# Kernel optimization log

Measured on AMD Instinct MI355X. Metric: run time of the kernel, lower is better.

## Reference

```python
import jax, jax.numpy as jnp
import numpy as np

B, N, E, H = 2048, 256, 32, 64
DIN = N + 2 * E  # masked_x + self_emb + parent_emb


def _lin_init(k, fan_in, fan_out):
    return jax.random.normal(k, (fan_in, fan_out), jnp.float32) / np.sqrt(fan_in).astype(np.float32)


def setup_inputs() -> dict:
    key = jax.random.key(0)
    ks = jax.random.split(key, 8)
    return {
        "x": jax.random.normal(ks[0], (B, N), jnp.float32),
        "adjacency": jax.random.uniform(ks[1], (N, N), jnp.float32),
        "embeddings": 0.01 * jax.random.normal(ks[2], (N, E), jnp.float32),
        "W1": _lin_init(ks[3], DIN, H), "b1": jnp.zeros((H,), jnp.float32),
        "g1": jnp.ones((H,), jnp.float32), "bt1": jnp.zeros((H,), jnp.float32),
        "W2": _lin_init(ks[4], H, H), "b2": jnp.zeros((H,), jnp.float32),
        "g2": jnp.ones((H,), jnp.float32), "bt2": jnp.zeros((H,), jnp.float32),
        "W3": _lin_init(ks[5], H, 2), "b3": jnp.zeros((2,), jnp.float32),
    }


def _layernorm(h, g, b, eps=1e-5):
    m = h.mean(-1, keepdims=True)
    v = h.var(-1, keepdims=True)
    return (h - m) / jnp.sqrt(v + eps) * g + b


def _leaky_relu(h):
    return jnp.where(h >= 0, h, 0.2 * h)


def reference(x, adjacency, embeddings, W1, b1, g1, bt1, W2, b2, g2, bt2, W3, b3):
    b, n = x.shape
    e = embeddings.shape[1]
    # masked_x[b,i,j] = adjacency[j,i] * x[b,j]  (per-node parent masking, vectorized over i)
    masked = x[:, None, :] * adjacency.T[None, :, :]            # (B, N, N)
    self_emb = jnp.broadcast_to(embeddings[None], (b, n, e))    # (B, N, E)
    # parent_weights[:, i] = adjacency[:, i] / (sum + 1e-8); parent_emb_i = pw_i @ embeddings
    pw = adjacency / (adjacency.sum(axis=0, keepdims=True) + 1e-8)
    parent_emb = jnp.broadcast_to((pw.T @ embeddings)[None], (b, n, e))  # (B, N, E)
    inp = jnp.concatenate([masked, self_emb, parent_emb], axis=-1)       # (B, N, N+2E)
    h = _leaky_relu(_layernorm(inp @ W1 + b1, g1, bt1))
    h = _leaky_relu(_layernorm(h @ W2 + b2, g2, bt2))
    out = h @ W3 + b3                                            # (B, N, 2)
    return out[..., 0], out[..., 1]  # (means, log_stds), each (B, N)
```

## Files before the change

### kernel.cpp

```cpp
#include <hip/hip_runtime.h>
#include <hip/hip_bf16.h>

#define BB 2048
#define NN 256
#define EE 32
#define HH 64

typedef __attribute__((ext_vector_type(8))) short s16x8;
typedef __attribute__((ext_vector_type(4))) short s16x4;
typedef __attribute__((ext_vector_type(4))) float f32x4;

__device__ __forceinline__ unsigned short f32_to_bf16_rne(float f) {
    unsigned int u = __float_as_uint(f);
    unsigned int r = u + 0x7FFFu + ((u >> 16) & 1u);
    return (unsigned short)(r >> 16);
}
__device__ __forceinline__ float bf16_to_f32(unsigned short h) {
    return __uint_as_float(((unsigned int)h) << 16);
}

__global__ void prep_x(const float* __restrict__ x,
                       unsigned short* __restrict__ xh,
                       unsigned short* __restrict__ xl) {
    const int i4 = (blockIdx.x * 256 + threadIdx.x) * 4;
    const f32x4 v = *(const f32x4*)(x + i4);
    s16x4 hv, lv;
    #pragma unroll
    for (int q = 0; q < 4; ++q) {
        const unsigned short hb = f32_to_bf16_rne(v[q]);
        hv[q] = (short)hb;
        lv[q] = (short)f32_to_bf16_rne(v[q] - bf16_to_f32(hb));
    }
    *(s16x4*)(xh + i4) = hv;
    *(s16x4*)(xl + i4) = lv;
}

__global__ __launch_bounds__(256) void precompute_c(
    const float* __restrict__ A, const float* __restrict__ emb,
    const float* __restrict__ W1, const float* __restrict__ b1,
    float* __restrict__ c) {
    const int i = blockIdx.x;
    const int t = threadIdx.x;
    __shared__ float aS[NN];
    __shared__ float red[256];
    __shared__ float peS[EE];

    const float a_t = A[t * NN + i];
    aS[t] = a_t;
    red[t] = a_t;
    __syncthreads();
    #pragma unroll
    for (int s = 128; s > 0; s >>= 1) {
        if (t < s) red[t] += red[t + s];
        __syncthreads();
    }
    const float inv = 1.f / (red[0] + 1e-8f);

    const int e = t & 31, jg = t >> 5;
    float part = 0.f;
    #pragma unroll 8
    for (int r = 0; r < 32; ++r) {
        const int j = jg * 32 + r;
        part = fmaf(aS[j], emb[j * EE + e], part);
    }
    __syncthreads();
    red[t] = part;
    __syncthreads();
    if (t < 32) {
        float pe = 0.f;
        #pragma unroll
        for (int g = 0; g < 8; ++g) pe += red[g * 32 + t];
        peS[t] = pe * inv;
    }
    __syncthreads();

    if (t < HH) {
        float ch = b1[t];
        const float* embi = emb + i * EE;
        #pragma unroll 8
        for (int e2 = 0; e2 < EE; ++e2) {
            ch = fmaf(embi[e2], W1[(NN      + e2) * HH + t], ch);
            ch = fmaf(peS[e2],  W1[(NN + EE + e2) * HH + t], ch);
        }
        c[i * HH + t] = ch;
    }
}

__global__ __launch_bounds__(256, 2) void fused_main(
    const unsigned short* __restrict__ xh, const unsigned short* __restrict__ xl,
    const float* __restrict__ A, const float* __restrict__ W1,
    const float* __restrict__ c,
    const float* __restrict__ g1, const float* __restrict__ bt1,
    const float* __restrict__ W2, const float* __restrict__ b2,
    const float* __restrict__ g2, const float* __restrict__ bt2,
    const float* __restrict__ W3, const float* __restrict__ b3,
    float* __restrict__ out) {

    __shared__ float smem[16384];
    __shared__ float aS[NN];
    unsigned short* Bh = (unsigned short*)smem;
    unsigned short* Bl = Bh + 32 * 512;
    float* h1 = smem;

    const int t  = threadIdx.x;
    const int i  = blockIdx.x & 255;
    const int b0 = (blockIdx.x >> 8) * 256;

    const int l  = t & 63;
    const int wv = t >> 6;
    const int lg = l >> 4;
    const int lm = l & 15;

    aS[t] = A[t * NN + i];
    __syncthreads();

    #pragma unroll
    for (int fr = 0; fr < 8; ++fr) {
        const int frag = wv * 8 + fr;
        const int kb = frag >> 2, nt = frag & 3;
        const int h  = nt * 16 + lm;
        const int jb = kb * 32 + lg * 8;
        s16x8 hv, lv;
        #pragma unroll
        for (int w = 0; w < 8; ++w) {
            const int j = jb + w;
            const float p = aS[j] * W1[j * HH + h];
            const unsigned short hb = f32_to_bf16_rne(p);
            hv[w] = (short)hb;
            lv[w] = (short)f32_to_bf16_rne(p - bf16_to_f32(hb));
        }
        *(s16x8*)(Bh + frag * 512 + l * 8) = hv;
        *(s16x8*)(Bl + frag * 512 + l * 8) = lv;
    }
    __syncthreads();

    f32x4 acc[4][4];
    #pragma unroll
    for (int rt = 0; rt < 4; ++rt)
        #pragma unroll
        for (int nt = 0; nt < 4; ++nt) {
            acc[rt][nt][0] = 0.f; acc[rt][nt][1] = 0.f;
            acc[rt][nt][2] = 0.f; acc[rt][nt][3] = 0.f;
        }

    const int rowbase = b0 + wv * 64;
    for (int kb = 0; kb < 8; ++kb) {
        s16x8 bh[4], bl[4];
        #pragma unroll
        for (int nt = 0; nt < 4; ++nt) {
            const int sbase = ((kb * 4 + nt) * 64 + l) * 8;
            bh[nt] = *(const s16x8*)(Bh + sbase);
            bl[nt] = *(const s16x8*)(Bl + sbase);
        }
        const int koff = kb * 32 + lg * 8;
        #pragma unroll
        for (int rt = 0; rt < 4; ++rt) {
            const int row = rowbase + rt * 16 + lm;
            const s16x8 ah = *(const s16x8*)(xh + row * NN + koff);
            const s16x8 al = *(const s16x8*)(xl + row * NN + koff);
            #pragma unroll
            for (int nt = 0; nt < 4; ++nt) {
                acc[rt][nt] = __builtin_amdgcn_mfma_f32_16x16x32_bf16(ah, bh[nt], acc[rt][nt], 0, 0, 0);
                acc[rt][nt] = __builtin_amdgcn_mfma_f32_16x16x32_bf16(ah, bl[nt], acc[rt][nt], 0, 0, 0);
                acc[rt][nt] = __builtin_amdgcn_mfma_f32_16x16x32_bf16(al, bh[nt], acc[rt][nt], 0, 0, 0);
            }
        }
    }
    __syncthreads();

    #pragma unroll
    for (int rt = 0; rt < 4; ++rt) {
        #pragma unroll
        for (int nt = 0; nt < 4; ++nt) {
            #pragma unroll
            for (int rr = 0; rr < 4; ++rr) {
                const int wr  = wv * 64 + rt * 16 + lg * 4 + rr;
                const int col = nt * 16 + lm;
                const int q   = col >> 2;
                h1[wr * 64 + (((q ^ (wr & 15)) << 2) | (col & 3))] = acc[rt][nt][rr];
            }
        }
    }
    __syncthreads();

    float acc1[HH];
    #pragma unroll
    for (int q = 0; q < 16; ++q) {
        const f32x4 v = *(const f32x4*)&h1[t * 64 + ((q ^ (t & 15)) << 2)];
        acc1[4*q+0] = v[0]; acc1[4*q+1] = v[1]; acc1[4*q+2] = v[2]; acc1[4*q+3] = v[3];
    }

    {
        const float* crow = c + i * HH;
        #pragma unroll
        for (int h = 0; h < HH; ++h) acc1[h] += crow[h];
    }

    {
        float m0 = 0.f, m1 = 0.f, m2 = 0.f, m3 = 0.f;
        #pragma unroll
        for (int h = 0; h < HH; h += 4) { m0 += acc1[h]; m1 += acc1[h+1]; m2 += acc1[h+2]; m3 += acc1[h+3]; }
        const float m = (m0 + m1 + m2 + m3) * (1.f / HH);
        float v0 = 0.f, v1 = 0.f, v2 = 0.f, v3 = 0.f;
        #pragma unroll
        for (int h = 0; h < HH; h += 4) {
            float d0 = acc1[h] - m, d1 = acc1[h+1] - m, d2 = acc1[h+2] - m, d3 = acc1[h+3] - m;
            v0 = fmaf(d0, d0, v0); v1 = fmaf(d1, d1, v1); v2 = fmaf(d2, d2, v2); v3 = fmaf(d3, d3, v3);
        }
        const float var = (v0 + v1 + v2 + v3) * (1.f / HH);
        const float inv = rsqrtf(var + 1e-5f);
        #pragma unroll
        for (int h = 0; h < HH; ++h) {
            float u = (acc1[h] - m) * inv * g1[h] + bt1[h];
            acc1[h] = (u >= 0.f) ? u : 0.2f * u;
        }
    }

    float acc2[HH];
    #pragma unroll
    for (int ho = 0; ho < HH; ++ho) acc2[ho] = b2[ho];
    #pragma unroll
    for (int h = 0; h < HH; ++h) {
        const float v = acc1[h];
        const float* w = W2 + h * HH;
        #pragma unroll
        for (int ho = 0; ho < HH; ++ho) acc2[ho] = fmaf(v, w[ho], acc2[ho]);
    }

    {
        float m0 = 0.f, m1 = 0.f, m2 = 0.f, m3 = 0.f;
        #pragma unroll
        for (int h = 0; h < HH; h += 4) { m0 += acc2[h]; m1 += acc2[h+1]; m2 += acc2[h+2]; m3 += acc2[h+3]; }
        const float m = (m0 + m1 + m2 + m3) * (1.f / HH);
        float v0 = 0.f, v1 = 0.f, v2 = 0.f, v3 = 0.f;
        #pragma unroll
        for (int h = 0; h < HH; h += 4) {
            float d0 = acc2[h] - m, d1 = acc2[h+1] - m, d2 = acc2[h+2] - m, d3 = acc2[h+3] - m;
            v0 = fmaf(d0, d0, v0); v1 = fmaf(d1, d1, v1); v2 = fmaf(d2, d2, v2); v3 = fmaf(d3, d3, v3);
        }
        const float var = (v0 + v1 + v2 + v3) * (1.f / HH);
        const float inv = rsqrtf(var + 1e-5f);
        #pragma unroll
        for (int h = 0; h < HH; ++h) {
            float u = (acc2[h] - m) * inv * g2[h] + bt2[h];
            acc2[h] = (u >= 0.f) ? u : 0.2f * u;
        }
    }

    float o0 = b3[0], o1 = b3[1];
    #pragma unroll
    for (int h = 0; h < HH; ++h) {
        o0 = fmaf(acc2[h], W3[h * 2 + 0], o0);
        o1 = fmaf(acc2[h], W3[h * 2 + 1], o1);
    }

    const int row = (b0 + t) * NN + i;
    out[row] = o0;
    out[BB * NN + row] = o1;
}

extern "C" void kernel_launch(void* const* d_in, const int* in_sizes, int n_in,
                              void* d_out, int out_size, void* d_ws, size_t ws_size,
                              hipStream_t stream) {
    const float* x   = (const float*)d_in[0];
    const float* A   = (const float*)d_in[1];
    const float* emb = (const float*)d_in[2];
    const float* W1  = (const float*)d_in[3];
    const float* b1  = (const float*)d_in[4];
    const float* g1  = (const float*)d_in[5];
    const float* bt1 = (const float*)d_in[6];
    const float* W2  = (const float*)d_in[7];
    const float* b2  = (const float*)d_in[8];
    const float* g2  = (const float*)d_in[9];
    const float* bt2 = (const float*)d_in[10];
    const float* W3  = (const float*)d_in[11];
    const float* b3  = (const float*)d_in[12];
    float* out = (float*)d_out;

    float* c = (float*)d_ws;
    unsigned short* xhp = (unsigned short*)(c + NN * HH);
    unsigned short* xlp = xhp + BB * NN;

    prep_x<<<(BB * NN) / 1024, 256, 0, stream>>>(x, xhp, xlp);
    precompute_c<<<NN, 256, 0, stream>>>(A, emb, W1, b1, c);
    fused_main<<<NN * (BB / 256), 256, 0, stream>>>(
        xhp, xlp, A, W1, c, g1, bt1, W2, b2, g2, bt2, W3, b3, out);
}
```

Measured before the change: 236.1 us.

## Split first GEMM into two 32-column halves to halve LDS and raise occupancy

The first-layer MFMA GEMM now runs in two passes over 32-column halves of the hidden dimension instead of one pass over all 64. This halves the shared-memory buffer and the per-thread accumulator tile, and the launch bounds go from 2 to 4 blocks per CU. The aim is more resident waves to hide the global loads of x. In exchange the xh/xl row tiles are loaded twice and there are extra barriers per block, and acc1[64] still adds register pressure that may cause spills under the tighter bound.

Result: slower. 379.1 us (+60.6%).

```diff
diff --git a/kernel.cpp b/kernel.cpp
--- a/kernel.cpp
+++ b/kernel.cpp
@@ -86,7 +86,7 @@
     }
 }
 
-__global__ __launch_bounds__(256, 2) void fused_main(
+__global__ __launch_bounds__(256, 4) void fused_main(
     const unsigned short* __restrict__ xh, const unsigned short* __restrict__ xl,
     const float* __restrict__ A, const float* __restrict__ W1,
     const float* __restrict__ c,
@@ -96,11 +96,11 @@
     const float* __restrict__ W3, const float* __restrict__ b3,
     float* __restrict__ out) {
 
-    __shared__ float smem[16384];
+    __shared__ float smem[8192];
     __shared__ float aS[NN];
     unsigned short* Bh = (unsigned short*)smem;
-    unsigned short* Bl = Bh + 32 * 512;
-    float* h1 = smem;
+    unsigned short* Bl = Bh + 16 * 512;
+    float* tr = smem;
 
     const int t  = threadIdx.x;
     const int i  = blockIdx.x & 255;
@@ -114,80 +114,86 @@
     aS[t] = A[t * NN + i];
     __syncthreads();
 
-    #pragma unroll
-    for (int fr = 0; fr < 8; ++fr) {
-        const int frag = wv * 8 + fr;
-        const int kb = frag >> 2, nt = frag & 3;
-        const int h  = nt * 16 + lm;
-        const int jb = kb * 32 + lg * 8;
-        s16x8 hv, lv;
-        #pragma unroll
-        for (int w = 0; w < 8; ++w) {
-            const int j = jb + w;
-            const float p = aS[j] * W1[j * HH + h];
-            const unsigned short hb = f32_to_bf16_rne(p);
-            hv[w] = (short)hb;
-            lv[w] = (short)f32_to_bf16_rne(p - bf16_to_f32(hb));
-        }
-        *(s16x8*)(Bh + frag * 512 + l * 8) = hv;
-        *(s16x8*)(Bl + frag * 512 + l * 8) = lv;
-    }
-    __syncthreads();
-
-    f32x4 acc[4][4];
-    #pragma unroll
-    for (int rt = 0; rt < 4; ++rt)
-        #pragma unroll
-        for (int nt = 0; nt < 4; ++nt) {
-            acc[rt][nt][0] = 0.f; acc[rt][nt][1] = 0.f;
-            acc[rt][nt][2] = 0.f; acc[rt][nt][3] = 0.f;
-        }
-
-    const int rowbase = b0 + wv * 64;
-    for (int kb = 0; kb < 8; ++kb) {
-        s16x8 bh[4], bl[4];
-        #pragma unroll
-        for (int nt = 0; nt < 4; ++nt) {
-            const int sbase = ((kb * 4 + nt) * 64 + l) * 8;
-            bh[nt] = *(const s16x8*)(Bh + sbase);
-            bl[nt] = *(const s16x8*)(Bl + sbase);
-        }
-        const int koff = kb * 32 + lg * 8;
+    float acc1[HH];
+
+    #pragma unroll
+    for (int p = 0; p < 2; ++p) {
+        #pragma unroll
+        for (int fr = 0; fr < 4; ++fr) {
+            const int f   = wv * 4 + fr;
+            const int kb  = f >> 1, ntl = f & 1;
+            const int h   = p * 32 + ntl * 16 + lm;
+            const int jb  = kb * 32 + lg * 8;
+            s16x8 hv, lv;
+            #pragma unroll
+            for (int w = 0; w < 8; ++w) {
+                const int j = jb + w;
+                const float pw = aS[j] * W1[j * HH + h];
+                const unsigned short hb = f32_to_bf16_rne(pw);
+                hv[w] = (short)hb;
+                lv[w] = (short)f32_to_bf16_rne(pw - bf16_to_f32(hb));
+            }
+            *(s16x8*)(Bh + f * 512 + l * 8) = hv;
+            *(s16x8*)(Bl + f * 512 + l * 8) = lv;
+        }
+        __syncthreads();
+
+        f32x4 acc[4][2];
+        #pragma unroll
+        for (int rt = 0; rt < 4; ++rt)
+            #pragma unroll
+            for (int n = 0; n < 2; ++n) {
+                acc[rt][n][0] = 0.f; acc[rt][n][1] = 0.f;
+                acc[rt][n][2] = 0.f; acc[rt][n][3] = 0.f;
+            }
+
+        const int rowbase = b0 + wv * 64;
+        for (int kb = 0; kb < 8; ++kb) {
+            s16x8 bh[2], bl[2];
+            #pragma unroll
+            for (int n = 0; n < 2; ++n) {
+                const int sbase = ((kb * 2 + n) * 64 + l) * 8;
+                bh[n] = *(const s16x8*)(Bh + sbase);
+                bl[n] = *(const s16x8*)(Bl + sbase);
+            }
+            const int koff = kb * 32 + lg * 8;
+            #pragma unroll
+            for (int rt = 0; rt < 4; ++rt) {
+                const int row = rowbase + rt * 16 + lm;
+                const s16x8 ah = *(const s16x8*)(xh + row * NN + koff);
+                const s16x8 al = *(const s16x8*)(xl + row * NN + koff);
+                #pragma unroll
+                for (int n = 0; n < 2; ++n) {
+                    acc[rt][n] = __builtin_amdgcn_mfma_f32_16x16x32_bf16(ah, bh[n], acc[rt][n], 0, 0, 0);
+                    acc[rt][n] = __builtin_amdgcn_mfma_f32_16x16x32_bf16(ah, bl[n], acc[rt][n], 0, 0, 0);
+                    acc[rt][n] = __builtin_amdgcn_mfma_f32_16x16x32_bf16(al, bh[n], acc[rt][n], 0, 0, 0);
+                }
+            }
+        }
+        __syncthreads();
+
         #pragma unroll
         for (int rt = 0; rt < 4; ++rt) {
-            const int row = rowbase + rt * 16 + lm;
-            const s16x8 ah = *(const s16x8*)(xh + row * NN + koff);
-            const s16x8 al = *(const s16x8*)(xl + row * NN + koff);
-            #pragma unroll
-            for (int nt = 0; nt < 4; ++nt) {
-                acc[rt][nt] = __builtin_amdgcn_mfma_f32_16x16x32_bf16(ah, bh[nt], acc[rt][nt], 0, 0, 0);
-                acc[rt][nt] = __builtin_amdgcn_mfma_f32_16x16x32_bf16(ah, bl[nt], acc[rt][nt], 0, 0, 0);
-                acc[rt][nt] = __builtin_amdgcn_mfma_f32_16x16x32_bf16(al, bh[nt], acc[rt][nt], 0, 0, 0);
-            }
-        }
-    }
-    __syncthreads();
-
-    #pragma unroll
-    for (int rt = 0; rt < 4; ++rt) {
-        #pragma unroll
-        for (int nt = 0; nt < 4; ++nt) {
-            #pragma unroll
-            for (int rr = 0; rr < 4; ++rr) {
-                const int wr  = wv * 64 + rt * 16 + lg * 4 + rr;
-                const int col = nt * 16 + lm;
-                const int q   = col >> 2;
-                h1[wr * 64 + (((q ^ (wr & 15)) << 2) | (col & 3))] = acc[rt][nt][rr];
-            }
-        }
-    }
-    __syncthreads();
-
-    float acc1[HH];
-    #pragma unroll
-    for (int q = 0; q < 16; ++q) {
-        const f32x4 v = *(const f32x4*)&h1[t * 64 + ((q ^ (t & 15)) << 2)];
-        acc1[4*q+0] = v[0]; acc1[4*q+1] = v[1]; acc1[4*q+2] = v[2]; acc1[4*q+3] = v[3];
+            #pragma unroll
+            for (int n = 0; n < 2; ++n) {
+                #pragma unroll
+                for (int rr = 0; rr < 4; ++rr) {
+                    const int wr  = wv * 64 + rt * 16 + lg * 4 + rr;
+                    const int col = n * 16 + lm;
+                    const int q   = col >> 2;
+                    tr[wr * 32 + (((q ^ (wr & 7)) << 2) | (col & 3))] = acc[rt][n][rr];
+                }
+            }
+        }
+        __syncthreads();
+
+        #pragma unroll
+        for (int g = 0; g < 8; ++g) {
+            const f32x4 v = *(const f32x4*)&tr[t * 32 + ((g ^ (t & 7)) << 2)];
+            acc1[p*32 + 4*g + 0] = v[0]; acc1[p*32 + 4*g + 1] = v[1];
+            acc1[p*32 + 4*g + 2] = v[2]; acc1[p*32 + 4*g + 3] = v[3];
+        }
+        __syncthreads();
     }
 
     {
```

## Move second-layer GEMM onto bf16 split-precision MFMA via shared-memory staging

Applied to the files above, without the earlier changes.

The per-thread scalar FP32 64x64 W2 matmul is replaced with MFMA bf16 hi/lo split (three products) computation. Layer-1 activations are split into bf16 hi/lo and written to LDS in MFMA fragment layout. A new prep kernel transposes and splits W2 once per call. The per-row LayerNorm epilogue is kept by transposing the accumulators back through LDS, which adds extra syncs and LDS traffic and slightly changes rounding.

Result: faster. 196.8 us (-16.6%).

```diff
diff --git a/kernel.cpp b/kernel.cpp
--- a/kernel.cpp
+++ b/kernel.cpp
@@ -33,6 +33,17 @@
     }
     *(s16x4*)(xh + i4) = hv;
     *(s16x4*)(xl + i4) = lv;
+}
+
+__global__ void prep_w2t(const float* __restrict__ W2,
+                         unsigned short* __restrict__ w2h,
+                         unsigned short* __restrict__ w2l) {
+    const int idx = blockIdx.x * 256 + threadIdx.x;
+    const int n = idx >> 6, k = idx & 63;
+    const float w = W2[k * HH + n];
+    const unsigned short hb = f32_to_bf16_rne(w);
+    w2h[n * HH + k] = hb;
+    w2l[n * HH + k] = f32_to_bf16_rne(w - bf16_to_f32(hb));
 }
 
 __global__ __launch_bounds__(256) void precompute_c(
@@ -90,8 +101,9 @@
     const unsigned short* __restrict__ xh, const unsigned short* __restrict__ xl,
     const float* __restrict__ A, const float* __restrict__ W1,
     const float* __restrict__ c,
+    const unsigned short* __restrict__ w2h, const unsigned short* __restrict__ w2l,
     const float* __restrict__ g1, const float* __restrict__ bt1,
-    const float* __restrict__ W2, const float* __restrict__ b2,
+    const float* __restrict__ b2,
     const float* __restrict__ g2, const float* __restrict__ bt2,
     const float* __restrict__ W3, const float* __restrict__ b3,
     float* __restrict__ out) {
@@ -100,7 +112,9 @@
     __shared__ float aS[NN];
     unsigned short* Bh = (unsigned short*)smem;
     unsigned short* Bl = Bh + 32 * 512;
-    float* h1 = smem;
+    float* tr = smem;
+    unsigned short* Ah = (unsigned short*)smem;
+    unsigned short* Al = Ah + 32 * 512;
 
     const int t  = threadIdx.x;
     const int i  = blockIdx.x & 255;
@@ -116,21 +130,21 @@
 
     #pragma unroll
     for (int fr = 0; fr < 8; ++fr) {
-        const int frag = wv * 8 + fr;
-        const int kb = frag >> 2, nt = frag & 3;
+        const int f  = wv * 8 + fr;
+        const int kb = f >> 2, nt = f & 3;
         const int h  = nt * 16 + lm;
         const int jb = kb * 32 + lg * 8;
         s16x8 hv, lv;
         #pragma unroll
         for (int w = 0; w < 8; ++w) {
             const int j = jb + w;
-            const float p = aS[j] * W1[j * HH + h];
-            const unsigned short hb = f32_to_bf16_rne(p);
+            const float pw = aS[j] * W1[j * HH + h];
+            const unsigned short hb = f32_to_bf16_rne(pw);
             hv[w] = (short)hb;
-            lv[w] = (short)f32_to_bf16_rne(p - bf16_to_f32(hb));
-        }
-        *(s16x8*)(Bh + frag * 512 + l * 8) = hv;
-        *(s16x8*)(Bl + frag * 512 + l * 8) = lv;
+            lv[w] = (short)f32_to_bf16_rne(pw - bf16_to_f32(hb));
+        }
+        *(s16x8*)(Bh + f * 512 + l * 8) = hv;
+        *(s16x8*)(Bl + f * 512 + l * 8) = lv;
     }
     __syncthreads();
 
@@ -169,33 +183,31 @@
     __syncthreads();
 
     #pragma unroll
-    for (int rt = 0; rt < 4; ++rt) {
-        #pragma unroll
-        for (int nt = 0; nt < 4; ++nt) {
+    for (int rt = 0; rt < 4; ++rt)
+        #pragma unroll
+        for (int nt = 0; nt < 4; ++nt)
             #pragma unroll
             for (int rr = 0; rr < 4; ++rr) {
                 const int wr  = wv * 64 + rt * 16 + lg * 4 + rr;
                 const int col = nt * 16 + lm;
                 const int q   = col >> 2;
-                h1[wr * 64 + (((q ^ (wr & 15)) << 2) | (col & 3))] = acc[rt][nt][rr];
-            }
-        }
-    }
+                tr[wr * 64 + (((q ^ (wr & 15)) << 2) | (col & 3))] = acc[rt][nt][rr];
+            }
     __syncthreads();
 
     float acc1[HH];
     #pragma unroll
     for (int q = 0; q < 16; ++q) {
-        const f32x4 v = *(const f32x4*)&h1[t * 64 + ((q ^ (t & 15)) << 2)];
+        const f32x4 v = *(const f32x4*)&tr[t * 64 + ((q ^ (t & 15)) << 2)];
         acc1[4*q+0] = v[0]; acc1[4*q+1] = v[1]; acc1[4*q+2] = v[2]; acc1[4*q+3] = v[3];
     }
+    __syncthreads();
 
     {
         const float* crow = c + i * HH;
         #pragma unroll
         for (int h = 0; h < HH; ++h) acc1[h] += crow[h];
     }
-
     {
         float m0 = 0.f, m1 = 0.f, m2 = 0.f, m3 = 0.f;
         #pragma unroll
@@ -216,42 +228,106 @@
         }
     }
 
-    float acc2[HH];
-    #pragma unroll
-    for (int ho = 0; ho < HH; ++ho) acc2[ho] = b2[ho];
-    #pragma unroll
-    for (int h = 0; h < HH; ++h) {
-        const float v = acc1[h];
-        const float* w = W2 + h * HH;
-        #pragma unroll
-        for (int ho = 0; ho < HH; ++ho) acc2[ho] = fmaf(v, w[ho], acc2[ho]);
-    }
+    {
+        const int f2base = (t >> 4) * 2;
+        const int lm2    = t & 15;
+        #pragma unroll
+        for (int w = 0; w < 8; ++w) {
+            const int kk = w >> 2, lg2 = w & 3;
+            s16x8 hv, lv;
+            #pragma unroll
+            for (int e = 0; e < 8; ++e) {
+                const float v = acc1[w * 8 + e];
+                const unsigned short hb = f32_to_bf16_rne(v);
+                hv[e] = (short)hb;
+                lv[e] = (short)f32_to_bf16_rne(v - bf16_to_f32(hb));
+            }
+            const int base = (f2base + kk) * 512 + (lg2 * 16 + lm2) * 8;
+            *(s16x8*)(Ah + base) = hv;
+            *(s16x8*)(Al + base) = lv;
+        }
+    }
+    __syncthreads();
+
+    f32x4 acc2[4][4];
+    #pragma unroll
+    for (int rt = 0; rt < 4; ++rt)
+        #pragma unroll
+        for (int nt = 0; nt < 4; ++nt) {
+            acc2[rt][nt][0] = 0.f; acc2[rt][nt][1] = 0.f;
+            acc2[rt][nt][2] = 0.f; acc2[rt][nt][3] = 0.f;
+        }
+    #pragma unroll
+    for (int kk = 0; kk < 2; ++kk) {
+        s16x8 b2h[4], b2l[4];
+        #pragma unroll
+        for (int nt = 0; nt < 4; ++nt) {
+            const int off = (nt * 16 + lm) * HH + kk * 32 + lg * 8;
+            b2h[nt] = *(const s16x8*)(w2h + off);
+            b2l[nt] = *(const s16x8*)(w2l + off);
+        }
+        #pragma unroll
+        for (int rt = 0; rt < 4; ++rt) {
+            const int base = ((wv * 4 + rt) * 2 + kk) * 512 + l * 8;
+            const s16x8 a2h = *(const s16x8*)(Ah + base);
+            const s16x8 a2l = *(const s16x8*)(Al + base);
+            #pragma unroll
+            for (int nt = 0; nt < 4; ++nt) {
+                acc2[rt][nt] = __builtin_amdgcn_mfma_f32_16x16x32_bf16(a2h, b2h[nt], acc2[rt][nt], 0, 0, 0);
+                acc2[rt][nt] = __builtin_amdgcn_mfma_f32_16x16x32_bf16(a2h, b2l[nt], acc2[rt][nt], 0, 0, 0);
+                acc2[rt][nt] = __builtin_amdgcn_mfma_f32_16x16x32_bf16(a2l, b2h[nt], acc2[rt][nt], 0, 0, 0);
+            }
+        }
+    }
+    __syncthreads();
+
+    #pragma unroll
+    for (int rt = 0; rt < 4; ++rt)
+        #pragma unroll
+        for (int nt = 0; nt < 4; ++nt)
+            #pragma unroll
+            for (int rr = 0; rr < 4; ++rr) {
+                const int wr  = wv * 64 + rt * 16 + lg * 4 + rr;
+                const int col = nt * 16 + lm;
+                const int q   = col >> 2;
+                tr[wr * 64 + (((q ^ (wr & 15)) << 2) | (col & 3))] = acc2[rt][nt][rr];
+            }
+    __syncthreads();
+
+    float accE[HH];
+    #pragma unroll
+    for (int q = 0; q < 16; ++q) {
+        const f32x4 v = *(const f32x4*)&tr[t * 64 + ((q ^ (t & 15)) << 2)];
+        accE[4*q+0] = v[0]; accE[4*q+1] = v[1]; accE[4*q+2] = v[2]; accE[4*q+3] = v[3];
+    }
+    #pragma unroll
+    for (int h = 0; h < HH; ++h) accE[h] += b2[h];
 
     {
         float m0 = 0.f, m1 = 0.f, m2 = 0.f, m3 = 0.f;
         #pragma unroll
-        for (int h = 0; h < HH; h += 4) { m0 += acc2[h]; m1 += acc2[h+1]; m2 += acc2[h+2]; m3 += acc2[h+3]; }
+        for (int h = 0; h < HH; h += 4) { m0 += accE[h]; m1 += accE[h+1]; m2 += accE[h+2]; m3 += accE[h+3]; }
         const float m = (m0 + m1 + m2 + m3) * (1.f / HH);
         float v0 = 0.f, v1 = 0.f, v2 = 0.f, v3 = 0.f;
         #pragma unroll
         for (int h = 0; h < HH; h += 4) {
-            float d0 = acc2[h] - m, d1 = acc2[h+1] - m, d2 = acc2[h+2] - m, d3 = acc2[h+3] - m;
+            float d0 = accE[h] - m, d1 = accE[h+1] - m, d2 = accE[h+2] - m, d3 = accE[h+3] - m;
             v0 = fmaf(d0, d0, v0); v1 = fmaf(d1, d1, v1); v2 = fmaf(d2, d2, v2); v3 = fmaf(d3, d3, v3);
         }
         const float var = (v0 + v1 + v2 + v3) * (1.f / HH);
         const float inv = rsqrtf(var + 1e-5f);
         #pragma unroll
         for (int h = 0; h < HH; ++h) {
-            float u = (acc2[h] - m) * inv * g2[h] + bt2[h];
-            acc2[h] = (u >= 0.f) ? u : 0.2f * u;
+            float u = (accE[h] - m) * inv * g2[h] + bt2[h];
+            accE[h] = (u >= 0.f) ? u : 0.2f * u;
         }
     }
 
     float o0 = b3[0], o1 = b3[1];
     #pragma unroll
     for (int h = 0; h < HH; ++h) {
-        o0 = fmaf(acc2[h], W3[h * 2 + 0], o0);
-        o1 = fmaf(acc2[h], W3[h * 2 + 1], o1);
+        o0 = fmaf(accE[h], W3[h * 2 + 0], o0);
+        o1 = fmaf(accE[h], W3[h * 2 + 1], o1);
     }
 
     const int row = (b0 + t) * NN + i;
@@ -280,9 +356,12 @@
     float* c = (float*)d_ws;
     unsigned short* xhp = (unsigned short*)(c + NN * HH);
     unsigned short* xlp = xhp + BB * NN;
+    unsigned short* w2hp = xlp + BB * NN;
+    unsigned short* w2lp = w2hp + HH * HH;
 
     prep_x<<<(BB * NN) / 1024, 256, 0, stream>>>(x, xhp, xlp);
+    prep_w2t<<<16, 256, 0, stream>>>(W2, w2hp, w2lp);
     precompute_c<<<NN, 256, 0, stream>>>(A, emb, W1, b1, c);
     fused_main<<<NN * (BB / 256), 256, 0, stream>>>(
-        xhp, xlp, A, W1, c, g1, bt1, W2, b2, g2, bt2, W3, b3, out);
-}
+        xhp, xlp, A, W1, c, w2hp, w2lp, g1, bt1, b2, g2, bt2, W3, b3, out);
+}
```
